# Performance work log

Measured on AMD Instinct MI355X. Metric: run time of the kernel, lower is better.

Reference implementation:

```python
import jax, jax.numpy as jnp
import numpy as np

NHEADS = 16

def setup_inputs() -> dict:
    key = jax.random.key(0)
    ks = jax.random.split(key, 11)
    B, S, D = 2, 2048, 1024
    std = 1.0 / np.sqrt(D)
    return {
        "query": jax.random.normal(ks[0], (B, S, D), jnp.float32),
        "key":   jax.random.normal(ks[1], (B, S, D), jnp.float32),
        "value": jax.random.normal(ks[2], (B, S, D), jnp.float32),
        "Wq": jax.random.normal(ks[3], (D, D), jnp.float32) * std,
        "bq": jax.random.normal(ks[4], (D,), jnp.float32) * std,
        "Wk": jax.random.normal(ks[5], (D, D), jnp.float32) * std,
        "bk": jax.random.normal(ks[6], (D,), jnp.float32) * std,
        "Wv": jax.random.normal(ks[7], (D, D), jnp.float32) * std,
        "bv": jax.random.normal(ks[8], (D,), jnp.float32) * std,
        "Wo": jax.random.normal(ks[9], (D, D), jnp.float32) * std,
        "bo": jax.random.normal(ks[10], (D,), jnp.float32) * std,
    }

def reference(query, key, value, Wq, bq, Wk, bk, Wv, bv, Wo, bo):
    B, Sq, D = query.shape
    Sk = key.shape[1]
    H = NHEADS
    hd = D // H
    q = (query @ Wq + bq).reshape(B, Sq, H, hd)
    k = (key @ Wk + bk).reshape(B, Sk, H, hd)
    v = (value @ Wv + bv).reshape(B, Sk, H, hd)
    # Explicit [B,H,Sq,Sk] score tensor, as in the original
    score = jnp.einsum('bqhd,bkhd->bhqk', q, k)
    # masked=True: causal mask applied before scaling (equivalent: -inf/c = -inf)
    cmask = jnp.triu(jnp.ones((Sq, Sk), dtype=bool), k=1)
    score = jnp.where(cmask, -jnp.inf, score)
    # NOTE: original divides by sqrt(score.shape[-1]) == sqrt(Sk), NOT sqrt(head_dim)
    scale = jnp.float32(1.0 / np.sqrt(Sk))
    att = jax.nn.softmax(score * scale, axis=-1)
    ret = jnp.einsum('bhqk,bkhd->bqhd', att, v).reshape(B, Sq, D)
    return ret @ Wo + bo
```

## Files before the change

kernel.cpp:

```cpp
#include <hip/hip_runtime.h>
#include <stdint.h>

typedef unsigned short u16;
typedef unsigned int u32;
typedef __bf16 bf16x8 __attribute__((ext_vector_type(8)));
typedef __bf16 bf16x4 __attribute__((ext_vector_type(4)));
typedef float f32x4 __attribute__((ext_vector_type(4)));

__device__ __forceinline__ u16 f2bf(float f) {
  u32 u = __float_as_uint(f);
  u = (u + 0x7fffu + ((u >> 16) & 1u)) >> 16;
  return (u16)u;
}

__device__ __forceinline__ void gload16(const void* g, void* l) {
  __builtin_amdgcn_global_load_lds(
      (const __attribute__((address_space(1))) void*)g,
      (__attribute__((address_space(3))) void*)l, 16, 0, 0);
}

__global__ __launch_bounds__(256) void cvt_qkv(
    const float* __restrict__ q, const float* __restrict__ k,
    const float* __restrict__ v, u16* __restrict__ dst) {
  const float* s = (blockIdx.y == 0) ? q : (blockIdx.y == 1) ? k : v;
  u16* d = dst + (size_t)blockIdx.y * 4194304u;
  int e = (blockIdx.x * 256 + threadIdx.x) * 8;
  float4 a = *(const float4*)(s + e);
  float4 b = *(const float4*)(s + e + 4);
  uint4 o;
  o.x = (u32)f2bf(a.x) | ((u32)f2bf(a.y) << 16);
  o.y = (u32)f2bf(a.z) | ((u32)f2bf(a.w) << 16);
  o.z = (u32)f2bf(b.x) | ((u32)f2bf(b.y) << 16);
  o.w = (u32)f2bf(b.z) | ((u32)f2bf(b.w) << 16);
  *(uint4*)(d + e) = o;
}

__global__ __launch_bounds__(512) void trans_w(
    const float* __restrict__ w0, const float* __restrict__ w1,
    const float* __restrict__ w2, const float* __restrict__ w3,
    u16* __restrict__ wt) {
  const float* W = (blockIdx.z == 0) ? w0 : (blockIdx.z == 1) ? w1
                   : (blockIdx.z == 2) ? w2 : w3;
  u16* Wt = wt + (size_t)blockIdx.z * 1048576u;
  __shared__ float tile[64][65];
  int x0 = blockIdx.x * 64, y0 = blockIdx.y * 64;
  int tx = threadIdx.x, ty = threadIdx.y;
#pragma unroll
  for (int j = 0; j < 8; ++j)
    tile[ty + j * 8][tx] = W[(size_t)(y0 + ty + j * 8) * 1024 + x0 + tx];
  __syncthreads();
#pragma unroll
  for (int j = 0; j < 8; ++j)
    Wt[(size_t)(x0 + ty + j * 8) * 1024 + y0 + tx] = f2bf(tile[tx][ty + j * 8]);
}

__global__ __launch_bounds__(256, 2) void gemm_proj(
    const u16* __restrict__ Xb, const u16* __restrict__ Wt,
    const float* __restrict__ bqp, const float* __restrict__ bkp,
    const float* __restrict__ bvp,
    u16* __restrict__ Qb, u16* __restrict__ Kb, u16* __restrict__ VtG,
    float qsc) {
  const int z = blockIdx.z;
  const u16 *A, *Bt;
  const float* bias;
  u16* C;
  int N, bm, bn;
  float osc = 1.f;
  bool rowb = false;
  if (z < 2) {
    A = Xb + (size_t)z * 4194304u;
    Bt = Wt + (size_t)z * 1048576u;
    bias = z ? bkp : bqp;
    C = z ? Kb : Qb;
    N = 1024;
    bm = blockIdx.x * 128;
    bn = blockIdx.y * 128;
    if (z == 0) osc = qsc;
  } else {
    A = Wt + 2u * 1048576u;
    Bt = Xb + 2u * 4194304u;
    bias = bvp;
    C = VtG;
    N = 4096;
    bm = blockIdx.y * 128;
    bn = blockIdx.x * 128;
    rowb = true;
  }

  __shared__ __align__(16) u16 ldsA[128 * 64];
  __shared__ __align__(16) u16 ldsB[128 * 64];

  const int tid = threadIdx.x;
  const int lane = tid & 63, wv = tid >> 6;
  const int wr = wv >> 1, wc = wv & 1;
  const int l15 = lane & 15, l4 = lane >> 4;

  const f32x4 zero4 = {0.f, 0.f, 0.f, 0.f};
  f32x4 acc[4][4];
#pragma unroll
  for (int i = 0; i < 4; ++i)
#pragma unroll
    for (int j = 0; j < 4; ++j) acc[i][j] = zero4;

  for (int kt = 0; kt < 16; ++kt) {
    __syncthreads();
#pragma unroll
    for (int g = 0; g < 4; ++g) {
      int p = g * 256 + tid;
      int row = p >> 3;
      int ss = (p & 7) ^ (row & 7);
      gload16(A + (size_t)(bm + row) * 1024 + kt * 64 + ss * 8,
              (char*)ldsA + (g * 256 + wv * 64) * 16);
    }
#pragma unroll
    for (int g = 0; g < 4; ++g) {
      int p = g * 256 + tid;
      int row = p >> 3;
      int ss = (p & 7) ^ (row & 7);
      gload16(Bt + (size_t)(bn + row) * 1024 + kt * 64 + ss * 8,
              (char*)ldsB + (g * 256 + wv * 64) * 16);
    }
    __syncthreads();

    bf16x8 af[4][2], bfr[4][2];
#pragma unroll
    for (int mf = 0; mf < 4; ++mf) {
      int row = wr * 64 + mf * 16 + l15;
#pragma unroll
      for (int ks = 0; ks < 2; ++ks) {
        int byt = row * 128 + ((ks * 64 + l4 * 16) ^ ((row & 7) << 4));
        af[mf][ks] = *(const bf16x8*)((const char*)ldsA + byt);
      }
    }
#pragma unroll
    for (int nf = 0; nf < 4; ++nf) {
      int row = wc * 64 + nf * 16 + l15;
#pragma unroll
      for (int ks = 0; ks < 2; ++ks) {
        int byt = row * 128 + ((ks * 64 + l4 * 16) ^ ((row & 7) << 4));
        bfr[nf][ks] = *(const bf16x8*)((const char*)ldsB + byt);
      }
    }
#pragma unroll
    for (int mf = 0; mf < 4; ++mf)
#pragma unroll
      for (int nf = 0; nf < 4; ++nf) {
        acc[mf][nf] = __builtin_amdgcn_mfma_f32_16x16x32_bf16(
            af[mf][0], bfr[nf][0], acc[mf][nf], 0, 0, 0);
        acc[mf][nf] = __builtin_amdgcn_mfma_f32_16x16x32_bf16(
            af[mf][1], bfr[nf][1], acc[mf][nf], 0, 0, 0);
      }
  }

  float bcol[4];
  if (!rowb) {
#pragma unroll
    for (int nf = 0; nf < 4; ++nf)
      bcol[nf] = bias[bn + wc * 64 + nf * 16 + l15];
  }
#pragma unroll
  for (int mf = 0; mf < 4; ++mf) {
#pragma unroll
    for (int i = 0; i < 4; ++i) {
      int r = bm + wr * 64 + mf * 16 + l4 * 4 + i;
      float br = rowb ? bias[r] : 0.f;
#pragma unroll
      for (int nf = 0; nf < 4; ++nf) {
        int c = bn + wc * 64 + nf * 16 + l15;
        float val = (acc[mf][nf][i] + (rowb ? br : bcol[nf])) * osc;
        C[(size_t)r * N + c] = f2bf(val);
      }
    }
  }
}

__global__ __launch_bounds__(256, 2) void gemm_out(
    const u16* __restrict__ A, const u16* __restrict__ Bt,
    const float* __restrict__ bias, float* __restrict__ C) {
  __shared__ __align__(16) u16 ldsA[128 * 64];
  __shared__ __align__(16) u16 ldsB[128 * 64];

  const int tid = threadIdx.x;
  const int lane = tid & 63, wv = tid >> 6;
  const int wr = wv >> 1, wc = wv & 1;
  const int l15 = lane & 15, l4 = lane >> 4;
  const int bm = blockIdx.x * 128, bn = blockIdx.y * 128;

  const f32x4 zero4 = {0.f, 0.f, 0.f, 0.f};
  f32x4 acc[4][4];
#pragma unroll
  for (int i = 0; i < 4; ++i)
#pragma unroll
    for (int j = 0; j < 4; ++j) acc[i][j] = zero4;

  for (int kt = 0; kt < 16; ++kt) {
    __syncthreads();
#pragma unroll
    for (int g = 0; g < 4; ++g) {
      int p = g * 256 + tid;
      int row = p >> 3;
      int ss = (p & 7) ^ (row & 7);
      gload16(A + (size_t)(bm + row) * 1024 + kt * 64 + ss * 8,
              (char*)ldsA + (g * 256 + wv * 64) * 16);
    }
#pragma unroll
    for (int g = 0; g < 4; ++g) {
      int p = g * 256 + tid;
      int row = p >> 3;
      int ss = (p & 7) ^ (row & 7);
      gload16(Bt + (size_t)(bn + row) * 1024 + kt * 64 + ss * 8,
              (char*)ldsB + (g * 256 + wv * 64) * 16);
    }
    __syncthreads();

    bf16x8 af[4][2], bfr[4][2];
#pragma unroll
    for (int mf = 0; mf < 4; ++mf) {
      int row = wr * 64 + mf * 16 + l15;
#pragma unroll
      for (int ks = 0; ks < 2; ++ks) {
        int byt = row * 128 + ((ks * 64 + l4 * 16) ^ ((row & 7) << 4));
        af[mf][ks] = *(const bf16x8*)((const char*)ldsA + byt);
      }
    }
#pragma unroll
    for (int nf = 0; nf < 4; ++nf) {
      int row = wc * 64 + nf * 16 + l15;
#pragma unroll
      for (int ks = 0; ks < 2; ++ks) {
        int byt = row * 128 + ((ks * 64 + l4 * 16) ^ ((row & 7) << 4));
        bfr[nf][ks] = *(const bf16x8*)((const char*)ldsB + byt);
      }
    }
#pragma unroll
    for (int mf = 0; mf < 4; ++mf)
#pragma unroll
      for (int nf = 0; nf < 4; ++nf) {
        acc[mf][nf] = __builtin_amdgcn_mfma_f32_16x16x32_bf16(
            af[mf][0], bfr[nf][0], acc[mf][nf], 0, 0, 0);
        acc[mf][nf] = __builtin_amdgcn_mfma_f32_16x16x32_bf16(
            af[mf][1], bfr[nf][1], acc[mf][nf], 0, 0, 0);
      }
  }

  float bcol[4];
#pragma unroll
  for (int nf = 0; nf < 4; ++nf)
    bcol[nf] = bias[bn + wc * 64 + nf * 16 + l15];
#pragma unroll
  for (int mf = 0; mf < 4; ++mf) {
#pragma unroll
    for (int i = 0; i < 4; ++i) {
      int r = bm + wr * 64 + mf * 16 + l4 * 4 + i;
#pragma unroll
      for (int nf = 0; nf < 4; ++nf) {
        int c = bn + wc * 64 + nf * 16 + l15;
        C[(size_t)r * 1024 + c] = acc[mf][nf][i] + bcol[nf];
      }
    }
  }
}

__global__ __launch_bounds__(256, 4) void attn_k(
    const u16* __restrict__ Q, const u16* __restrict__ Kb,
    const u16* __restrict__ Vt, u16* __restrict__ ctx) {
  const int id = blockIdx.x + (blockIdx.y << 5);
  const int xcd = id & 7;
  const int kk = id >> 3;
  const int bh = xcd * 4 + (kk & 3);
  const int qt = 31 - (kk >> 2);
  const int b = bh >> 4, h = bh & 15;
  const int tid = threadIdx.x;
  const int lane = tid & 63, wv = tid >> 6;
  const int l15 = lane & 15, l4 = lane >> 4;

  __shared__ __align__(16) u16 Kt[2][64 * 64];
  __shared__ __align__(16) u16 Vl[2][64 * 64];
  __shared__ __align__(16) u16 Pl[4][16 * 64];

  const u16* KB = Kb + (size_t)(b * 2048) * 1024 + h * 64;
  const u16* VB = Vt + (size_t)(h * 64) * 4096 + b * 2048;

  const u16* qp =
      Q + (size_t)(b * 2048 + qt * 64 + wv * 16 + l15) * 1024 + h * 64;
  bf16x8 qf0 = *(const bf16x8*)(qp + l4 * 8);
  bf16x8 qf1 = *(const bf16x8*)(qp + 32 + l4 * 8);

  const f32x4 zero4 = {0.f, 0.f, 0.f, 0.f};
  f32x4 oacc[4];
#pragma unroll
  for (int i = 0; i < 4; ++i) oacc[i] = zero4;
  float m = -1e30f, lsum = 0.f;

  auto issueKV = [&](int jt, int bufi) {
    const u16* kb = KB + (size_t)(jt * 64) * 1024;
#pragma unroll
    for (int g = 0; g < 2; ++g) {
      int p = g * 256 + tid;
      int row = p >> 3;
      int ss = (p & 7) ^ (row & 7);
      gload16(kb + (size_t)row * 1024 + ss * 8,
              (char*)(&Kt[bufi][0]) + (g * 256 + wv * 64) * 16);
    }
#pragma unroll
    for (int g = 0; g < 2; ++g) {
      int p = g * 256 + tid;
      int d = p >> 3;
      int ss = (p & 7) ^ (d & 7);
      gload16(VB + (size_t)d * 4096 + jt * 64 + ss * 8,
              (char*)(&Vl[bufi][0]) + (g * 256 + wv * 64) * 16);
    }
  };

  issueKV(0, 0);
  for (int j = 0; j <= qt; ++j) {
    const int cur = j & 1;
    __syncthreads();
    if (j < qt) issueKV(j + 1, cur ^ 1);

    f32x4 p4[4];
    __builtin_amdgcn_s_setprio(1);
#pragma unroll
    for (int nt = 0; nt < 4; ++nt) {
      int row = nt * 16 + l15;
      int sw = (row & 7) << 4;
      const char* kr = (const char*)&Kt[cur][0] + row * 128;
      bf16x8 k0 = *(const bf16x8*)(kr + ((l4 * 16) ^ sw));
      bf16x8 k1 = *(const bf16x8*)(kr + ((64 + l4 * 16) ^ sw));
      f32x4 s = zero4;
      s = __builtin_amdgcn_mfma_f32_16x16x32_bf16(k0, qf0, s, 0, 0, 0);
      s = __builtin_amdgcn_mfma_f32_16x16x32_bf16(k1, qf1, s, 0, 0, 0);
      p4[nt] = s;
    }
    __builtin_amdgcn_s_setprio(0);

    if (j == qt) {
#pragma unroll
      for (int nt = 0; nt < 4; ++nt)
#pragma unroll
        for (int i = 0; i < 4; ++i)
          if (nt * 16 + l4 * 4 + i > wv * 16 + l15) p4[nt][i] = -1e30f;
    }

    float rm = p4[0][0];
#pragma unroll
    for (int nt = 0; nt < 4; ++nt)
#pragma unroll
      for (int i = 0; i < 4; ++i) rm = fmaxf(rm, p4[nt][i]);
    rm = fmaxf(rm, __shfl_xor(rm, 16, 64));
    rm = fmaxf(rm, __shfl_xor(rm, 32, 64));

    if (!__all(rm - m <= 8.0f)) {
      float mn = fmaxf(m, rm);
      float ce = exp2f(m - mn);
      m = mn;
      lsum *= ce;
#pragma unroll
      for (int i = 0; i < 4; ++i) {
        float cei = __shfl(ce, (lane & 48) | (l4 * 4 + i), 64);
#pragma unroll
        for (int nt = 0; nt < 4; ++nt) oacc[nt][i] *= cei;
      }
    }

    float rs = 0.f;
#pragma unroll
    for (int nt = 0; nt < 4; ++nt)
#pragma unroll
      for (int i = 0; i < 4; ++i) {
        float e = exp2f(p4[nt][i] - m);
        p4[nt][i] = e;
        rs += e;
      }
    rs += __shfl_xor(rs, 16, 64);
    rs += __shfl_xor(rs, 32, 64);
    lsum += rs;

    {
      int sw = (l15 & 7) << 4;
#pragma unroll
      for (int nt = 0; nt < 4; ++nt) {
        bf16x4 pb = __builtin_convertvector(p4[nt], bf16x4);
        *(bf16x4*)((char*)&Pl[wv][0] + l15 * 128 + ((nt * 32 + l4 * 8) ^ sw)) = pb;
      }
    }

    bf16x8 pa0, pa1;
    {
      int sw = (l15 & 7) << 4;
      pa0 = *(const bf16x8*)((const char*)&Pl[wv][0] + l15 * 128 + ((l4 * 16) ^ sw));
      pa1 = *(const bf16x8*)((const char*)&Pl[wv][0] + l15 * 128 +
                             ((64 + l4 * 16) ^ sw));
    }
    __builtin_amdgcn_s_setprio(1);
#pragma unroll
    for (int nt = 0; nt < 4; ++nt) {
      int d = nt * 16 + l15;
      int sw = (d & 7) << 4;
      const char* vr = (const char*)&Vl[cur][0] + d * 128;
      bf16x8 v0 = *(const bf16x8*)(vr + ((l4 * 16) ^ sw));
      bf16x8 v1 = *(const bf16x8*)(vr + ((64 + l4 * 16) ^ sw));
      oacc[nt] = __builtin_amdgcn_mfma_f32_16x16x32_bf16(pa0, v0, oacc[nt], 0, 0, 0);
      oacc[nt] = __builtin_amdgcn_mfma_f32_16x16x32_bf16(pa1, v1, oacc[nt], 0, 0, 0);
    }
    __builtin_amdgcn_s_setprio(0);
  }

  float rcp = 1.f / lsum;
  u16* cb = ctx + (size_t)(b * 2048 + qt * 64 + wv * 16) * 1024 + h * 64;
#pragma unroll
  for (int i = 0; i < 4; ++i) {
    float iv = __shfl(rcp, (lane & 48) | (l4 * 4 + i), 64);
    int r = l4 * 4 + i;
#pragma unroll
    for (int nt = 0; nt < 4; ++nt)
      cb[(size_t)r * 1024 + nt * 16 + l15] = f2bf(oacc[nt][i] * iv);
  }
}

extern "C" void kernel_launch(void* const* d_in, const int* in_sizes, int n_in,
                              void* d_out, int out_size, void* d_ws,
                              size_t ws_size, hipStream_t stream) {
  const float* q  = (const float*)d_in[0];
  const float* k  = (const float*)d_in[1];
  const float* v  = (const float*)d_in[2];
  const float* Wq = (const float*)d_in[3];
  const float* bq = (const float*)d_in[4];
  const float* Wk = (const float*)d_in[5];
  const float* bk = (const float*)d_in[6];
  const float* Wv = (const float*)d_in[7];
  const float* bv = (const float*)d_in[8];
  const float* Wo = (const float*)d_in[9];
  const float* bo = (const float*)d_in[10];

  char* ws = (char*)d_ws;
  u16* Xb  = (u16*)ws;
  u16* Wt  = (u16*)(ws + 25165824);
  u16* VtG = (u16*)(ws + 33554432);
  u16* ctx = Xb;
  u16* Qb  = (u16*)d_out;
  u16* Kb  = Qb + 4194304;

  const float SC2A = 0.0318793585f;

  cvt_qkv<<<dim3(2048, 3), 256, 0, stream>>>(q, k, v, Xb);
  trans_w<<<dim3(16, 16, 4), dim3(64, 8), 0, stream>>>(Wq, Wk, Wv, Wo, Wt);
  gemm_proj<<<dim3(32, 8, 3), 256, 0, stream>>>(Xb, Wt, bq, bk, bv, Qb, Kb,
                                                VtG, SC2A);
  attn_k<<<dim3(32, 32), 256, 0, stream>>>(Qb, Kb, VtG, ctx);
  gemm_out<<<dim3(32, 8), 256, 0, stream>>>(ctx, Wt + 3 * 1048576, bo,
                                            (float*)d_out);
}
```

Baseline: 116.1 us.

## Double-buffer LDS tiles in projection GEMMs and tree-reduce softmax max/sum

Both GEMM kernels (QKV projection and output projection) now use two LDS buffers per operand. The next K-tile's global-to-LDS loads are issued right after the barrier, so they overlap the MFMA work on the current tile instead of stalling before each tile. The MFMA block runs at raised wave priority. In the attention kernel, the per-row max and sum reductions become balanced trees to shorten the serial dependency chains. Double buffering doubles LDS use per block, 64KB, which may reduce occupancy for the kernel declared with two blocks per CU.

```diff
diff --git a/kernel.cpp b/kernel.cpp
--- a/kernel.cpp
+++ b/kernel.cpp
@@ -87,8 +87,8 @@
     rowb = true;
   }
 
-  __shared__ __align__(16) u16 ldsA[128 * 64];
-  __shared__ __align__(16) u16 ldsB[128 * 64];
+  __shared__ __align__(16) u16 ldsA[2][128 * 64];
+  __shared__ __align__(16) u16 ldsB[2][128 * 64];
 
   const int tid = threadIdx.x;
   const int lane = tid & 63, wv = tid >> 6;
@@ -102,15 +102,14 @@
 #pragma unroll
     for (int j = 0; j < 4; ++j) acc[i][j] = zero4;
 
-  for (int kt = 0; kt < 16; ++kt) {
-    __syncthreads();
+  auto issueT = [&](int kt, int bufi) {
 #pragma unroll
     for (int g = 0; g < 4; ++g) {
       int p = g * 256 + tid;
       int row = p >> 3;
       int ss = (p & 7) ^ (row & 7);
       gload16(A + (size_t)(bm + row) * 1024 + kt * 64 + ss * 8,
-              (char*)ldsA + (g * 256 + wv * 64) * 16);
+              (char*)&ldsA[bufi][0] + (g * 256 + wv * 64) * 16);
     }
 #pragma unroll
     for (int g = 0; g < 4; ++g) {
@@ -118,9 +117,15 @@
       int row = p >> 3;
       int ss = (p & 7) ^ (row & 7);
       gload16(Bt + (size_t)(bn + row) * 1024 + kt * 64 + ss * 8,
-              (char*)ldsB + (g * 256 + wv * 64) * 16);
-    }
+              (char*)&ldsB[bufi][0] + (g * 256 + wv * 64) * 16);
+    }
+  };
+
+  issueT(0, 0);
+  for (int kt = 0; kt < 16; ++kt) {
+    const int cur = kt & 1;
     __syncthreads();
+    if (kt + 1 < 16) issueT(kt + 1, cur ^ 1);
 
     bf16x8 af[4][2], bfr[4][2];
 #pragma unroll
@@ -129,7 +134,7 @@
 #pragma unroll
       for (int ks = 0; ks < 2; ++ks) {
         int byt = row * 128 + ((ks * 64 + l4 * 16) ^ ((row & 7) << 4));
-        af[mf][ks] = *(const bf16x8*)((const char*)ldsA + byt);
+        af[mf][ks] = *(const bf16x8*)((const char*)&ldsA[cur][0] + byt);
       }
     }
 #pragma unroll
@@ -138,9 +143,10 @@
 #pragma unroll
       for (int ks = 0; ks < 2; ++ks) {
         int byt = row * 128 + ((ks * 64 + l4 * 16) ^ ((row & 7) << 4));
-        bfr[nf][ks] = *(const bf16x8*)((const char*)ldsB + byt);
-      }
-    }
+        bfr[nf][ks] = *(const bf16x8*)((const char*)&ldsB[cur][0] + byt);
+      }
+    }
+    __builtin_amdgcn_s_setprio(1);
 #pragma unroll
     for (int mf = 0; mf < 4; ++mf)
 #pragma unroll
@@ -150,6 +156,7 @@
         acc[mf][nf] = __builtin_amdgcn_mfma_f32_16x16x32_bf16(
             af[mf][1], bfr[nf][1], acc[mf][nf], 0, 0, 0);
       }
+    __builtin_amdgcn_s_setprio(0);
   }
 
   float bcol[4];
@@ -177,8 +184,8 @@
 __global__ __launch_bounds__(256, 2) void gemm_out(
     const u16* __restrict__ A, const u16* __restrict__ Bt,
     const float* __restrict__ bias, float* __restrict__ C) {
-  __shared__ __align__(16) u16 ldsA[128 * 64];
-  __shared__ __align__(16) u16 ldsB[128 * 64];
+  __shared__ __align__(16) u16 ldsA[2][128 * 64];
+  __shared__ __align__(16) u16 ldsB[2][128 * 64];
 
   const int tid = threadIdx.x;
   const int lane = tid & 63, wv = tid >> 6;
@@ -193,15 +200,14 @@
 #pragma unroll
     for (int j = 0; j < 4; ++j) acc[i][j] = zero4;
 
-  for (int kt = 0; kt < 16; ++kt) {
-    __syncthreads();
+  auto issueT = [&](int kt, int bufi) {
 #pragma unroll
     for (int g = 0; g < 4; ++g) {
       int p = g * 256 + tid;
       int row = p >> 3;
       int ss = (p & 7) ^ (row & 7);
       gload16(A + (size_t)(bm + row) * 1024 + kt * 64 + ss * 8,
-              (char*)ldsA + (g * 256 + wv * 64) * 16);
+              (char*)&ldsA[bufi][0] + (g * 256 + wv * 64) * 16);
     }
 #pragma unroll
     for (int g = 0; g < 4; ++g) {
@@ -209,9 +215,15 @@
       int row = p >> 3;
       int ss = (p & 7) ^ (row & 7);
       gload16(Bt + (size_t)(bn + row) * 1024 + kt * 64 + ss * 8,
-              (char*)ldsB + (g * 256 + wv * 64) * 16);
-    }
+              (char*)&ldsB[bufi][0] + (g * 256 + wv * 64) * 16);
+    }
+  };
+
+  issueT(0, 0);
+  for (int kt = 0; kt < 16; ++kt) {
+    const int cur = kt & 1;
     __syncthreads();
+    if (kt + 1 < 16) issueT(kt + 1, cur ^ 1);
 
     bf16x8 af[4][2], bfr[4][2];
 #pragma unroll
@@ -220,7 +232,7 @@
 #pragma unroll
       for (int ks = 0; ks < 2; ++ks) {
         int byt = row * 128 + ((ks * 64 + l4 * 16) ^ ((row & 7) << 4));
-        af[mf][ks] = *(const bf16x8*)((const char*)ldsA + byt);
+        af[mf][ks] = *(const bf16x8*)((const char*)&ldsA[cur][0] + byt);
       }
     }
 #pragma unroll
@@ -229,9 +241,10 @@
 #pragma unroll
       for (int ks = 0; ks < 2; ++ks) {
         int byt = row * 128 + ((ks * 64 + l4 * 16) ^ ((row & 7) << 4));
-        bfr[nf][ks] = *(const bf16x8*)((const char*)ldsB + byt);
-      }
-    }
+        bfr[nf][ks] = *(const bf16x8*)((const char*)&ldsB[cur][0] + byt);
+      }
+    }
+    __builtin_amdgcn_s_setprio(1);
 #pragma unroll
     for (int mf = 0; mf < 4; ++mf)
 #pragma unroll
@@ -241,6 +254,7 @@
         acc[mf][nf] = __builtin_amdgcn_mfma_f32_16x16x32_bf16(
             af[mf][1], bfr[nf][1], acc[mf][nf], 0, 0, 0);
       }
+    __builtin_amdgcn_s_setprio(0);
   }
 
   float bcol[4];
@@ -342,11 +356,11 @@
           if (nt * 16 + l4 * 4 + i > wv * 16 + l15) p4[nt][i] = -1e30f;
     }
 
-    float rm = p4[0][0];
-#pragma unroll
-    for (int nt = 0; nt < 4; ++nt)
-#pragma unroll
-      for (int i = 0; i < 4; ++i) rm = fmaxf(rm, p4[nt][i]);
+    float mx0 = fmaxf(fmaxf(p4[0][0], p4[0][1]), fmaxf(p4[0][2], p4[0][3]));
+    float mx1 = fmaxf(fmaxf(p4[1][0], p4[1][1]), fmaxf(p4[1][2], p4[1][3]));
+    float mx2 = fmaxf(fmaxf(p4[2][0], p4[2][1]), fmaxf(p4[2][2], p4[2][3]));
+    float mx3 = fmaxf(fmaxf(p4[3][0], p4[3][1]), fmaxf(p4[3][2], p4[3][3]));
+    float rm = fmaxf(fmaxf(mx0, mx1), fmaxf(mx2, mx3));
     rm = fmaxf(rm, __shfl_xor(rm, 16, 64));
     rm = fmaxf(rm, __shfl_xor(rm, 32, 64));
 
@@ -363,15 +377,15 @@
       }
     }
 
-    float rs = 0.f;
 #pragma unroll
     for (int nt = 0; nt < 4; ++nt)
 #pragma unroll
-      for (int i = 0; i < 4; ++i) {
-        float e = exp2f(p4[nt][i] - m);
-        p4[nt][i] = e;
-        rs += e;
-      }
+      for (int i = 0; i < 4; ++i) p4[nt][i] = exp2f(p4[nt][i] - m);
+    float s0 = (p4[0][0] + p4[0][1]) + (p4[0][2] + p4[0][3]);
+    float s1 = (p4[1][0] + p4[1][1]) + (p4[1][2] + p4[1][3]);
+    float s2 = (p4[2][0] + p4[2][1]) + (p4[2][2] + p4[2][3]);
+    float s3 = (p4[3][0] + p4[3][1]) + (p4[3][2] + p4[3][3]);
+    float rs = (s0 + s1) + (s2 + s3);
     rs += __shfl_xor(rs, 16, 64);
     rs += __shfl_xor(rs, 32, 64);
     lsum += rs;
```

New measurement: 126.7 us. 1.09x slower.

## Switch attention to 32x32 MFMA with register-resident P via permlane swap

Applied to the files above, without the earlier changes.

Rewrites the attention kernel to use 2 waves of 32 query rows each with 32x32x16 bf16 MFMAs instead of 4 waves of 16 rows with 16x16x32. The softmax probabilities stay in registers and are repacked into the PV operand layout with cvt_pk_bf16 and permlane32_swap, removing the LDS round trip for P. Row max and sum reductions need fewer shuffles, and the output rescale no longer needs per-row shuffles. The trade-off is fewer threads per block, higher register pressure from 16-wide accumulators, and more gload instructions per thread for the K/V tiles.

```diff
diff --git a/kernel.cpp b/kernel.cpp
--- a/kernel.cpp
+++ b/kernel.cpp
@@ -3,9 +3,11 @@
 
 typedef unsigned short u16;
 typedef unsigned int u32;
+typedef u32 u32x4 __attribute__((ext_vector_type(4)));
 typedef __bf16 bf16x8 __attribute__((ext_vector_type(8)));
 typedef __bf16 bf16x4 __attribute__((ext_vector_type(4)));
 typedef float f32x4 __attribute__((ext_vector_type(4)));
+typedef float f32x16 __attribute__((ext_vector_type(16)));
 
 __device__ __forceinline__ u16 f2bf(float f) {
   u32 u = __float_as_uint(f);
@@ -17,6 +19,16 @@
   __builtin_amdgcn_global_load_lds(
       (const __attribute__((address_space(1))) void*)g,
       (__attribute__((address_space(3))) void*)l, 16, 0, 0);
+}
+
+__device__ __forceinline__ u32 cvtpk(float a, float b) {
+  u32 r;
+  asm("v_cvt_pk_bf16_f32 %0, %1, %2" : "=v"(r) : "v"(a), "v"(b));
+  return r;
+}
+
+__device__ __forceinline__ void plswap(u32& x, u32& y) {
+  asm volatile("v_permlane32_swap_b32 %0, %1" : "+v"(x), "+v"(y));
 }
 
 __global__ __launch_bounds__(256) void cvt_qkv(
@@ -261,7 +273,7 @@
   }
 }
 
-__global__ __launch_bounds__(256, 4) void attn_k(
+__global__ __launch_bounds__(128, 2) void attn_k(
     const u16* __restrict__ Q, const u16* __restrict__ Kb,
     const u16* __restrict__ Vt, u16* __restrict__ ctx) {
   const int id = blockIdx.x + (blockIdx.y << 5);
@@ -272,45 +284,47 @@
   const int b = bh >> 4, h = bh & 15;
   const int tid = threadIdx.x;
   const int lane = tid & 63, wv = tid >> 6;
-  const int l15 = lane & 15, l4 = lane >> 4;
+  const int l31 = lane & 31, l4b = lane >> 5;
 
   __shared__ __align__(16) u16 Kt[2][64 * 64];
   __shared__ __align__(16) u16 Vl[2][64 * 64];
-  __shared__ __align__(16) u16 Pl[4][16 * 64];
 
   const u16* KB = Kb + (size_t)(b * 2048) * 1024 + h * 64;
   const u16* VB = Vt + (size_t)(h * 64) * 4096 + b * 2048;
 
-  const u16* qp =
-      Q + (size_t)(b * 2048 + qt * 64 + wv * 16 + l15) * 1024 + h * 64;
-  bf16x8 qf0 = *(const bf16x8*)(qp + l4 * 8);
-  bf16x8 qf1 = *(const bf16x8*)(qp + 32 + l4 * 8);
-
-  const f32x4 zero4 = {0.f, 0.f, 0.f, 0.f};
-  f32x4 oacc[4];
-#pragma unroll
-  for (int i = 0; i < 4; ++i) oacc[i] = zero4;
+  const int qrow = qt * 64 + wv * 32 + l31;
+  const u16* qp = Q + (size_t)(b * 2048 + qrow) * 1024 + h * 64;
+  bf16x8 qf[4];
+#pragma unroll
+  for (int ks = 0; ks < 4; ++ks)
+    qf[ks] = *(const bf16x8*)(qp + ks * 16 + l4b * 8);
+
+  const f32x16 z16 = {0.f, 0.f, 0.f, 0.f, 0.f, 0.f, 0.f, 0.f,
+                      0.f, 0.f, 0.f, 0.f, 0.f, 0.f, 0.f, 0.f};
+  f32x16 o0 = z16, o1 = z16;
   float m = -1e30f, lsum = 0.f;
 
   auto issueKV = [&](int jt, int bufi) {
     const u16* kb = KB + (size_t)(jt * 64) * 1024;
 #pragma unroll
-    for (int g = 0; g < 2; ++g) {
-      int p = g * 256 + tid;
+    for (int g = 0; g < 4; ++g) {
+      int p = g * 128 + tid;
       int row = p >> 3;
       int ss = (p & 7) ^ (row & 7);
       gload16(kb + (size_t)row * 1024 + ss * 8,
-              (char*)(&Kt[bufi][0]) + (g * 256 + wv * 64) * 16);
-    }
-#pragma unroll
-    for (int g = 0; g < 2; ++g) {
-      int p = g * 256 + tid;
+              (char*)(&Kt[bufi][0]) + (g * 128 + wv * 64) * 16);
+    }
+#pragma unroll
+    for (int g = 0; g < 4; ++g) {
+      int p = g * 128 + tid;
       int d = p >> 3;
       int ss = (p & 7) ^ (d & 7);
       gload16(VB + (size_t)d * 4096 + jt * 64 + ss * 8,
-              (char*)(&Vl[bufi][0]) + (g * 256 + wv * 64) * 16);
+              (char*)(&Vl[bufi][0]) + (g * 128 + wv * 64) * 16);
     }
   };
+
+  const int swz = (l31 & 7) << 4;
 
   issueKV(0, 0);
   for (int j = 0; j <= qt; ++j) {
@@ -318,36 +332,39 @@
     __syncthreads();
     if (j < qt) issueKV(j + 1, cur ^ 1);
 
-    f32x4 p4[4];
+    f32x16 p0 = z16, p1 = z16;
     __builtin_amdgcn_s_setprio(1);
 #pragma unroll
-    for (int nt = 0; nt < 4; ++nt) {
-      int row = nt * 16 + l15;
-      int sw = (row & 7) << 4;
-      const char* kr = (const char*)&Kt[cur][0] + row * 128;
-      bf16x8 k0 = *(const bf16x8*)(kr + ((l4 * 16) ^ sw));
-      bf16x8 k1 = *(const bf16x8*)(kr + ((64 + l4 * 16) ^ sw));
-      f32x4 s = zero4;
-      s = __builtin_amdgcn_mfma_f32_16x16x32_bf16(k0, qf0, s, 0, 0, 0);
-      s = __builtin_amdgcn_mfma_f32_16x16x32_bf16(k1, qf1, s, 0, 0, 0);
-      p4[nt] = s;
+    for (int ks = 0; ks < 4; ++ks) {
+      const char* k0r = (const char*)&Kt[cur][0] + l31 * 128;
+      const char* k1r = (const char*)&Kt[cur][0] + (32 + l31) * 128;
+      bf16x8 k0 = *(const bf16x8*)(k0r + ((ks * 32 + l4b * 16) ^ swz));
+      bf16x8 k1 = *(const bf16x8*)(k1r + ((ks * 32 + l4b * 16) ^ swz));
+      p0 = __builtin_amdgcn_mfma_f32_32x32x16_bf16(k0, qf[ks], p0, 0, 0, 0);
+      p1 = __builtin_amdgcn_mfma_f32_32x32x16_bf16(k1, qf[ks], p1, 0, 0, 0);
     }
     __builtin_amdgcn_s_setprio(0);
 
     if (j == qt) {
 #pragma unroll
-      for (int nt = 0; nt < 4; ++nt)
-#pragma unroll
-        for (int i = 0; i < 4; ++i)
-          if (nt * 16 + l4 * 4 + i > wv * 16 + l15) p4[nt][i] = -1e30f;
-    }
-
-    float rm = p4[0][0];
-#pragma unroll
-    for (int nt = 0; nt < 4; ++nt)
-#pragma unroll
-      for (int i = 0; i < 4; ++i) rm = fmaxf(rm, p4[nt][i]);
-    rm = fmaxf(rm, __shfl_xor(rm, 16, 64));
+      for (int r = 0; r < 16; ++r) {
+        int kvl = (r & 3) + 8 * (r >> 2) + 4 * l4b;
+        int kv = j * 64 + kvl;
+        if (kv > qrow) p0[r] = -1e30f;
+        if (kv + 32 > qrow) p1[r] = -1e30f;
+      }
+    }
+
+    float a0 = fmaxf(fmaxf(p0[0], p0[1]), fmaxf(p0[2], p0[3]));
+    float a1 = fmaxf(fmaxf(p0[4], p0[5]), fmaxf(p0[6], p0[7]));
+    float a2 = fmaxf(fmaxf(p0[8], p0[9]), fmaxf(p0[10], p0[11]));
+    float a3 = fmaxf(fmaxf(p0[12], p0[13]), fmaxf(p0[14], p0[15]));
+    float b0 = fmaxf(fmaxf(p1[0], p1[1]), fmaxf(p1[2], p1[3]));
+    float b1 = fmaxf(fmaxf(p1[4], p1[5]), fmaxf(p1[6], p1[7]));
+    float b2 = fmaxf(fmaxf(p1[8], p1[9]), fmaxf(p1[10], p1[11]));
+    float b3 = fmaxf(fmaxf(p1[12], p1[13]), fmaxf(p1[14], p1[15]));
+    float rm = fmaxf(fmaxf(fmaxf(a0, a1), fmaxf(a2, a3)),
+                     fmaxf(fmaxf(b0, b1), fmaxf(b2, b3)));
     rm = fmaxf(rm, __shfl_xor(rm, 32, 64));
 
     if (!__all(rm - m <= 8.0f)) {
@@ -356,65 +373,75 @@
       m = mn;
       lsum *= ce;
 #pragma unroll
-      for (int i = 0; i < 4; ++i) {
-        float cei = __shfl(ce, (lane & 48) | (l4 * 4 + i), 64);
-#pragma unroll
-        for (int nt = 0; nt < 4; ++nt) oacc[nt][i] *= cei;
+      for (int r = 0; r < 16; ++r) {
+        o0[r] *= ce;
+        o1[r] *= ce;
       }
     }
 
     float rs = 0.f;
 #pragma unroll
-    for (int nt = 0; nt < 4; ++nt)
-#pragma unroll
-      for (int i = 0; i < 4; ++i) {
-        float e = exp2f(p4[nt][i] - m);
-        p4[nt][i] = e;
-        rs += e;
-      }
-    rs += __shfl_xor(rs, 16, 64);
+    for (int r = 0; r < 16; ++r) {
+      float e0 = exp2f(p0[r] - m);
+      float e1 = exp2f(p1[r] - m);
+      p0[r] = e0;
+      p1[r] = e1;
+      rs += e0 + e1;
+    }
     rs += __shfl_xor(rs, 32, 64);
     lsum += rs;
 
+    bf16x8 pf[4];
+#pragma unroll
+    for (int ks = 0; ks < 4; ++ks) {
+      const int s = ks & 1;
+      u32 c0, c1, c2, c3;
+      if (ks < 2) {
+        c0 = cvtpk(p0[8 * s + 0], p0[8 * s + 1]);
+        c1 = cvtpk(p0[8 * s + 2], p0[8 * s + 3]);
+        c2 = cvtpk(p0[8 * s + 4], p0[8 * s + 5]);
+        c3 = cvtpk(p0[8 * s + 6], p0[8 * s + 7]);
+      } else {
+        c0 = cvtpk(p1[8 * s + 0], p1[8 * s + 1]);
+        c1 = cvtpk(p1[8 * s + 2], p1[8 * s + 3]);
+        c2 = cvtpk(p1[8 * s + 4], p1[8 * s + 5]);
+        c3 = cvtpk(p1[8 * s + 6], p1[8 * s + 7]);
+      }
+      plswap(c0, c2);
+      plswap(c1, c3);
+      u32x4 w = {c0, c1, c2, c3};
+      pf[ks] = __builtin_bit_cast(bf16x8, w);
+    }
+
+    __builtin_amdgcn_s_setprio(1);
+#pragma unroll
+    for (int ks = 0; ks < 4; ++ks) {
+      const char* v0r = (const char*)&Vl[cur][0] + l31 * 128;
+      const char* v1r = (const char*)&Vl[cur][0] + (32 + l31) * 128;
+      bf16x8 v0 = *(const bf16x8*)(v0r + ((ks * 32 + l4b * 16) ^ swz));
+      bf16x8 v1 = *(const bf16x8*)(v1r + ((ks * 32 + l4b * 16) ^ swz));
+      o0 = __builtin_amdgcn_mfma_f32_32x32x16_bf16(v0, pf[ks], o0, 0, 0, 0);
+      o1 = __builtin_amdgcn_mfma_f32_32x32x16_bf16(v1, pf[ks], o1, 0, 0, 0);
+    }
+    __builtin_amdgcn_s_setprio(0);
+  }
+
+  float rcp = 1.f / lsum;
+  u16* cb = ctx + (size_t)(b * 2048 + qrow) * 1024 + h * 64;
+#pragma unroll
+  for (int g = 0; g < 4; ++g) {
     {
-      int sw = (l15 & 7) << 4;
-#pragma unroll
-      for (int nt = 0; nt < 4; ++nt) {
-        bf16x4 pb = __builtin_convertvector(p4[nt], bf16x4);
-        *(bf16x4*)((char*)&Pl[wv][0] + l15 * 128 + ((nt * 32 + l4 * 8) ^ sw)) = pb;
-      }
-    }
-
-    bf16x8 pa0, pa1;
+      int d = 8 * g + 4 * l4b;
+      f32x4 t = {o0[4 * g + 0] * rcp, o0[4 * g + 1] * rcp,
+                 o0[4 * g + 2] * rcp, o0[4 * g + 3] * rcp};
+      *(bf16x4*)(cb + d) = __builtin_convertvector(t, bf16x4);
+    }
     {
-      int sw = (l15 & 7) << 4;
-      pa0 = *(const bf16x8*)((const char*)&Pl[wv][0] + l15 * 128 + ((l4 * 16) ^ sw));
-      pa1 = *(const bf16x8*)((const char*)&Pl[wv][0] + l15 * 128 +
-                             ((64 + l4 * 16) ^ sw));
-    }
-    __builtin_amdgcn_s_setprio(1);
-#pragma unroll
-    for (int nt = 0; nt < 4; ++nt) {
-      int d = nt * 16 + l15;
-      int sw = (d & 7) << 4;
-      const char* vr = (const char*)&Vl[cur][0] + d * 128;
-      bf16x8 v0 = *(const bf16x8*)(vr + ((l4 * 16) ^ sw));
-      bf16x8 v1 = *(const bf16x8*)(vr + ((64 + l4 * 16) ^ sw));
-      oacc[nt] = __builtin_amdgcn_mfma_f32_16x16x32_bf16(pa0, v0, oacc[nt], 0, 0, 0);
-      oacc[nt] = __builtin_amdgcn_mfma_f32_16x16x32_bf16(pa1, v1, oacc[nt], 0, 0, 0);
-    }
-    __builtin_amdgcn_s_setprio(0);
-  }
-
-  float rcp = 1.f / lsum;
-  u16* cb = ctx + (size_t)(b * 2048 + qt * 64 + wv * 16) * 1024 + h * 64;
-#pragma unroll
-  for (int i = 0; i < 4; ++i) {
-    float iv = __shfl(rcp, (lane & 48) | (l4 * 4 + i), 64);
-    int r = l4 * 4 + i;
-#pragma unroll
-    for (int nt = 0; nt < 4; ++nt)
-      cb[(size_t)r * 1024 + nt * 16 + l15] = f2bf(oacc[nt][i] * iv);
+      int d = 32 + 8 * g + 4 * l4b;
+      f32x4 t = {o1[4 * g + 0] * rcp, o1[4 * g + 1] * rcp,
+                 o1[4 * g + 2] * rcp, o1[4 * g + 3] * rcp};
+      *(bf16x4*)(cb + d) = __builtin_convertvector(t, bf16x4);
+    }
   }
 }
 
@@ -447,7 +474,7 @@
   trans_w<<<dim3(16, 16, 4), dim3(64, 8), 0, stream>>>(Wq, Wk, Wv, Wo, Wt);
   gemm_proj<<<dim3(32, 8, 3), 256, 0, stream>>>(Xb, Wt, bq, bk, bv, Qb, Kb,
                                                 VtG, SC2A);
-  attn_k<<<dim3(32, 32), 256, 0, stream>>>(Qb, Kb, VtG, ctx);
+  attn_k<<<dim3(32, 32), 128, 0, stream>>>(Qb, Kb, VtG, ctx);
   gemm_out<<<dim3(32, 8), 256, 0, stream>>>(ctx, Wt + 3 * 1048576, bo,
                                             (float*)d_out);
 }
```

New measurement: 128.7 us. 10.9% more time.
